# Kernel tuning notes

Hardware: AMD Instinct MI355X
Metric: run time of the kernel (lower is better)

## Reference

```python
import jax, jax.numpy as jnp
import numpy as np

HIDDEN = 896
NUM_Q_HEADS = 14
NUM_KV_HEADS = 2
HEAD_DIM = 64
ROPE_BASE = 10000.0
B, S = 4, 2048


def rotate_half(x):
    x1, x2 = jnp.split(x, 2, axis=-1)
    return jnp.concatenate((-x2, x1), axis=-1)


def rope_cos_sin(position_ids):
    # position_ids: [B, S] int -> cos/sin [B, 1, S, HEAD_DIM]
    inv_freq = 1.0 / (ROPE_BASE ** (jnp.arange(0, HEAD_DIM, 2, dtype=jnp.float32) / HEAD_DIM))
    freqs = position_ids.astype(jnp.float32)[..., None] * inv_freq  # [B,S,D/2]
    emb = jnp.concatenate((freqs, freqs), axis=-1)  # [B,S,D]
    return jnp.cos(emb)[:, None, :, :], jnp.sin(emb)[:, None, :, :]


def setup_inputs() -> dict:
    key = jax.random.key(0)
    k1, k2, k3, k4, k5 = jax.random.split(key, 5)
    s = 1.0 / np.sqrt(HIDDEN)
    return {
        "hidden_states": jax.random.normal(k1, (B, S, HIDDEN), dtype=jnp.float32),
        "position_ids": jnp.broadcast_to(jnp.arange(S, dtype=jnp.int64), (B, S)),
        "Wq": jax.random.normal(k2, (HIDDEN, NUM_Q_HEADS * HEAD_DIM), dtype=jnp.float32) * s,
        "Wk": jax.random.normal(k3, (HIDDEN, NUM_KV_HEADS * HEAD_DIM), dtype=jnp.float32) * s,
        "Wv": jax.random.normal(k4, (HIDDEN, NUM_KV_HEADS * HEAD_DIM), dtype=jnp.float32) * s,
        "Wo": jax.random.normal(k5, (NUM_Q_HEADS * HEAD_DIM, HIDDEN), dtype=jnp.float32) * s,
    }


def reference(hidden_states, position_ids, Wq, Wk, Wv, Wo):
    b, s, _ = hidden_states.shape
    n_rep = NUM_Q_HEADS // NUM_KV_HEADS

    q = (hidden_states @ Wq).reshape(b, s, NUM_Q_HEADS, HEAD_DIM).transpose(0, 2, 1, 3)   # [B,Hq,S,D]
    k = (hidden_states @ Wk).reshape(b, s, NUM_KV_HEADS, HEAD_DIM).transpose(0, 2, 1, 3)  # [B,Hkv,S,D]
    v = (hidden_states @ Wv).reshape(b, s, NUM_KV_HEADS, HEAD_DIM).transpose(0, 2, 1, 3)

    cos, sin = rope_cos_sin(position_ids)  # [B,1,S,D]
    q = q * cos + rotate_half(q) * sin
    k = k * cos + rotate_half(k) * sin

    # repeat_interleave KV heads to match query heads
    k = jnp.repeat(k, n_rep, axis=1)  # [B,Hq,S,D]
    v = jnp.repeat(v, n_rep, axis=1)

    scale = 1.0 / jnp.sqrt(jnp.float32(HEAD_DIM))
    attn = jnp.einsum('bhqd,bhkd->bhqk', q, k) * scale  # [B,Hq,S,S]
    attn = jax.nn.softmax(attn, axis=-1)
    out = jnp.einsum('bhqk,bhkd->bhqd', attn, v)  # [B,Hq,S,D]
    out = out.transpose(0, 2, 1, 3).reshape(b, s, NUM_Q_HEADS * HEAD_DIM)
    return out @ Wo
```

## Files before the change

### kernel.cpp

```cpp
#include <hip/hip_runtime.h>
#include <hip/hip_bf16.h>
#include <math.h>

typedef unsigned short ushort_t;
typedef __bf16 bf16x8 __attribute__((ext_vector_type(8)));
typedef float f32x4 __attribute__((ext_vector_type(4)));

#define HIDDEN 896
#define NQH 14
#define NKVH 2
#define HD 64
#define SEQ 2048
#define NBATCH 4

__device__ inline ushort_t f2bf(float x) {
  union { float f; unsigned u; } c; c.f = x;
  unsigned r = c.u + 0x7FFFu + ((c.u >> 16) & 1u);
  return (ushort_t)(r >> 16);
}

__device__ inline unsigned pack2bf(float a, float b) {
  union { float f; unsigned u; } ca, cb; ca.f = a; cb.f = b;
  unsigned ua = ca.u + 0x8000u, ub = cb.u + 0x8000u;
  return __builtin_amdgcn_perm(ub, ua, 0x07060302);
}

__device__ inline unsigned cvtpk(float a, float b) {
  unsigned r;
  asm("v_cvt_pk_bf16_f32 %0, %1, %2" : "=v"(r) : "v"(a), "v"(b));
  return r;
}

__device__ inline bf16x8 ldfrag(const ushort_t* p) {
  return *reinterpret_cast<const bf16x8*>(p);
}

__device__ inline void async16(const ushort_t* g, ushort_t* l) {
  __builtin_amdgcn_global_load_lds(
      (const __attribute__((address_space(1))) void*)g,
      (__attribute__((address_space(3))) void*)l, 16, 0, 0);
}


__device__ inline void transpose_sec(const float* __restrict__ in, ushort_t* __restrict__ out,
                                     int K, int N, int bx, int by) {
  __shared__ float tile[32][33];
  int k0 = by * 32, n0 = bx * 32;
  for (int r = threadIdx.y; r < 32; r += 8) {
    int k = k0 + r, n = n0 + threadIdx.x;
    tile[r][threadIdx.x] = (k < K && n < N) ? in[(size_t)k * N + n] : 0.f;
  }
  __syncthreads();
  for (int r = threadIdx.y; r < 32; r += 8) {
    int n = n0 + r, k = k0 + threadIdx.x;
    if (n < N && k < K) out[(size_t)n * K + k] = f2bf(tile[threadIdx.x][r]);
  }
}

__global__ void k_prep(const float* __restrict__ hidden, ushort_t* __restrict__ hb,
                       const float* __restrict__ Wq, const float* __restrict__ Wk,
                       const float* __restrict__ Wv, const float* __restrict__ Wo,
                       ushort_t* __restrict__ wT, ushort_t* __restrict__ woT,
                       float2* __restrict__ ctab) {
  const int blk = blockIdx.x;
  const int tid = threadIdx.y * 32 + threadIdx.x;
  if (blk < 7168) {
    int i = blk * 256 + tid;
    float4 v = reinterpret_cast<const float4*>(hidden)[i];
    ushort4 o;
    o.x = f2bf(v.x); o.y = f2bf(v.y); o.z = f2bf(v.z); o.w = f2bf(v.w);
    reinterpret_cast<ushort4*>(hb)[i] = o;
  } else if (blk < 7424) {
    int idx = (blk - 7168) * 256 + tid;
    int s = idx >> 5, dp = idx & 31;
    float inv = exp2f(-(float)dp * 0.41524101186092596f);
    float ang = (float)s * inv;
    float sn, cn;
    sincosf(ang, &sn, &cn);
    ctab[idx] = make_float2(cn, sn);
  } else if (blk < 8208) {
    int t = blk - 7424;
    transpose_sec(Wq, wT, 896, 896, t % 28, t / 28);
  } else if (blk < 8320) {
    int t = blk - 8208;
    transpose_sec(Wk, wT + (size_t)896 * 896, 896, 128, t % 4, t / 4);
  } else if (blk < 8432) {
    int t = blk - 8320;
    transpose_sec(Wv, wT + (size_t)1024 * 896, 896, 128, t % 4, t / 4);
  } else {
    int t = blk - 8432;
    transpose_sec(Wo, woT, 896, 896, t % 28, t / 28);
  }
}

__global__ __launch_bounds__(256) void k_qkv(
    const ushort_t* __restrict__ hb,
    const ushort_t* __restrict__ wT,
    const int* __restrict__ pos_ids,
    const float2* __restrict__ ctab,
    ushort_t* __restrict__ Qg,
    ushort_t* __restrict__ Kg,
    ushort_t* __restrict__ Vtg) {
  __shared__ ushort_t smem[12288];
  ushort_t* sa = smem;
  ushort_t* sbb = smem + 8192;

  const int f = blockIdx.x;
  const int x = f & 7, s8 = f >> 3;
  const int sect = s8 % 18;
  const int mt = (s8 / 18) * 8 + x;
  const int nt0 = sect * 64;
  const int m0 = mt * 128;
  const int tid = threadIdx.x;
  const int wave = tid >> 6, lane = tid & 63;
  const int l15 = lane & 15, quad = lane >> 4;
  const int sw = l15 & 7;

  f32x4 acc[2][4];
  const f32x4 z4 = {0.f, 0.f, 0.f, 0.f};
#pragma unroll
  for (int mm = 0; mm < 2; ++mm)
#pragma unroll
    for (int nb = 0; nb < 4; ++nb) acc[mm][nb] = z4;

  for (int kt = 0; kt < 14; ++kt) {
    const int k0 = kt * 64;
    __syncthreads();
#pragma unroll
    for (int i = 0; i < 4; ++i) {
      int id = i * 256 + tid;
      int row = id >> 3;
      int cs = (id & 7) ^ (row & 7);
      async16(hb + (size_t)(m0 + row) * HIDDEN + k0 + cs * 8, sa + (i * 256 + wave * 64) * 8);
    }
#pragma unroll
    for (int i = 0; i < 2; ++i) {
      int id = i * 256 + tid;
      int row = id >> 3;
      int cs = (id & 7) ^ (row & 7);
      async16(wT + (size_t)(nt0 + row) * HIDDEN + k0 + cs * 8, sbb + (i * 256 + wave * 64) * 8);
    }
    __syncthreads();
#pragma unroll
    for (int kc = 0; kc < 2; ++kc) {
      int c = kc * 4 + quad;
      bf16x8 af[2], bf[4];
#pragma unroll
      for (int mm = 0; mm < 2; ++mm)
        af[mm] = ldfrag(sa + ((wave * 32 + mm * 16 + l15) * 8 + (c ^ sw)) * 8);
#pragma unroll
      for (int nb = 0; nb < 4; ++nb)
        bf[nb] = ldfrag(sbb + ((nb * 16 + l15) * 8 + (c ^ sw)) * 8);
#pragma unroll
      for (int mm = 0; mm < 2; ++mm)
#pragma unroll
        for (int nb = 0; nb < 4; ++nb)
          acc[mm][nb] = __builtin_amdgcn_mfma_f32_16x16x32_bf16(af[mm], bf[nb], acc[mm][nb], 0, 0, 0);
    }
  }

  if (sect < 16) {
    const bool isQ = sect < 14;
    const float csc = isQ ? 0.125f * 1.4426950408889634f : 1.0f;
    ushort_t* dst = isQ ? Qg : Kg;
    const int nheads = isQ ? NQH : NKVH;
    const int hh = isQ ? sect : sect - 14;
#pragma unroll
    for (int mm = 0; mm < 2; ++mm) {
#pragma unroll
      for (int r = 0; r < 4; ++r) {
        int token = m0 + wave * 32 + mm * 16 + quad * 4 + r;
        int b = token >> 11, s = token & 2047;
        int pos = pos_ids[token];
        size_t base = ((size_t)(b * nheads + hh) * SEQ + s) * HD;
#pragma unroll
        for (int nb = 0; nb < 2; ++nb) {
          float2 cs = ctab[pos * 32 + nb * 16 + l15];
          float x0 = acc[mm][nb][r];
          float x1 = acc[mm][nb + 2][r];
          float y0 = (x0 * cs.x - x1 * cs.y) * csc;
          float y1 = (x1 * cs.x + x0 * cs.y) * csc;
          dst[base + nb * 16 + l15]      = f2bf(y0);
          dst[base + nb * 16 + l15 + 32] = f2bf(y1);
        }
      }
    }
  } else {
    const int kvh = sect - 16;
    __syncthreads();
    ushort_t* vt = smem;
#pragma unroll
    for (int mm = 0; mm < 2; ++mm) {
      int tl = wave * 32 + mm * 16 + quad * 4;
      int chunk = tl >> 3, ofs = tl & 7;
#pragma unroll
      for (int nb = 0; nb < 4; ++nb) {
        int row = nb * 16 + l15;
        int slot = chunk ^ (row & 7);
        ushort_t* p = vt + row * 128 + slot * 8 + ofs;
        *reinterpret_cast<unsigned*>(p)     = pack2bf(acc[mm][nb][0], acc[mm][nb][1]);
        *reinterpret_cast<unsigned*>(p + 2) = pack2bf(acc[mm][nb][2], acc[mm][nb][3]);
      }
    }
    __syncthreads();
    const int bb = m0 >> 11, s0 = m0 & 2047;
#pragma unroll
    for (int i = 0; i < 4; ++i) {
      int id = i * 256 + tid;
      int row = id >> 4, ch = id & 15;
      int slot = ch ^ (row & 7);
      uint4 v = *reinterpret_cast<const uint4*>(vt + row * 128 + slot * 8);
      *reinterpret_cast<uint4*>(Vtg + ((size_t)(bb * NKVH + kvh) * HD + row) * SEQ + s0 + ch * 8) = v;
    }
  }
}

__global__ __launch_bounds__(256) void k_attn(
    const ushort_t* __restrict__ Qg,
    const ushort_t* __restrict__ Kg,
    const ushort_t* __restrict__ Vtg,
    ushort_t* __restrict__ attn) {
  __shared__ ushort_t kbuf[2][32 * 64];
  __shared__ ushort_t vbuf[2][64 * 32];
  __shared__ ushort_t pbuf[4][32 * 40];

  const int f = blockIdx.x;
  const int x = f & 7, s8 = f >> 3;
  const int lh = s8 % 7;
  const int qt = s8 / 7;
  const int b = x >> 1, kvh = x & 1;
  const int h = kvh * 7 + lh;
  const int bh = b * NQH + h;
  const int tid = threadIdx.x;
  const int wave = tid >> 6, lane = tid & 63;
  const int l15 = lane & 15, quad = lane >> 4;
  const int q0 = qt * 128;

  bf16x8 qf[2][2];
#pragma unroll
  for (int qs = 0; qs < 2; ++qs) {
    const size_t qb = ((size_t)bh * SEQ + q0 + wave * 32 + qs * 16 + l15) * HD + quad * 8;
    qf[qs][0] = ldfrag(Qg + qb);
    qf[qs][1] = ldfrag(Qg + qb + 32);
  }

  const size_t kbase = (size_t)(b * NKVH + kvh) * SEQ * HD;
  const size_t vbase = (size_t)(b * NKVH + kvh) * HD * SEQ;

  const int krow = tid >> 3;
  const int kcs = (tid & 7) ^ (krow & 7);
  const int vrow = tid >> 2;
  const int vcs = (tid & 3) ^ ((vrow >> 1) & 3);
  const int sdst = wave * 512;

  const ushort_t* kg = Kg + kbase + (size_t)krow * HD + kcs * 8;
  const ushort_t* vg = Vtg + vbase + (size_t)vrow * SEQ + vcs * 8;

  float l_part[2] = {0.f, 0.f};
  f32x4 o[2][4];
  const f32x4 z4 = {0.f, 0.f, 0.f, 0.f};
#pragma unroll
  for (int qs = 0; qs < 2; ++qs)
#pragma unroll
    for (int nb = 0; nb < 4; ++nb) o[qs][nb] = z4;

  ushort_t* pw = pbuf[wave];

  auto stage = [&](ushort_t* kb, ushort_t* vb) {
    async16(kg, kb + sdst);
    async16(vg, vb + sdst);
    kg += 32 * HD;
    vg += 32;
  };

  auto compute = [&](const ushort_t* kb, const ushort_t* vb) {
#pragma unroll
    for (int nb = 0; nb < 2; ++nb) {
      int row = nb * 16 + l15;
      int swz = row & 7;
      bf16x8 kf0 = ldfrag(kb + (row * 8 + (quad ^ swz)) * 8);
      bf16x8 kf1 = ldfrag(kb + (row * 8 + ((4 + quad) ^ swz)) * 8);
#pragma unroll
      for (int qs = 0; qs < 2; ++qs) {
        f32x4 t = z4;
        t = __builtin_amdgcn_mfma_f32_16x16x32_bf16(kf0, qf[qs][0], t, 0, 0, 0);
        t = __builtin_amdgcn_mfma_f32_16x16x32_bf16(kf1, qf[qs][1], t, 0, 0, 0);
        float p0 = __builtin_amdgcn_exp2f(t[0]);
        float p1 = __builtin_amdgcn_exp2f(t[1]);
        float p2 = __builtin_amdgcn_exp2f(t[2]);
        float p3 = __builtin_amdgcn_exp2f(t[3]);
        l_part[qs] += (p0 + p1) + (p2 + p3);
        uint2 d;
        d.x = cvtpk(p0, p1);
        d.y = cvtpk(p2, p3);
        *reinterpret_cast<uint2*>(pw + (qs * 16 + l15) * 40 + nb * 16 + quad * 4) = d;
      }
    }

    bf16x8 pf[2];
#pragma unroll
    for (int qs = 0; qs < 2; ++qs)
      pf[qs] = ldfrag(pw + (qs * 16 + l15) * 40 + quad * 8);
#pragma unroll
    for (int nb = 0; nb < 4; ++nb) {
      int row = nb * 16 + l15;
      bf16x8 vf = ldfrag(vb + row * 32 + ((quad ^ ((row >> 1) & 3)) * 8));
#pragma unroll
      for (int qs = 0; qs < 2; ++qs)
        o[qs][nb] = __builtin_amdgcn_mfma_f32_16x16x32_bf16(pf[qs], vf, o[qs][nb], 0, 0, 0);
    }
  };

  stage(kbuf[0], vbuf[0]);
  asm volatile("s_waitcnt vmcnt(0)" ::: "memory");
  __builtin_amdgcn_s_barrier();
  __builtin_amdgcn_sched_barrier(0);

  for (int jt = 0; jt < 62; jt += 2) {
    stage(kbuf[1], vbuf[1]);
    compute(kbuf[0], vbuf[0]);
    __builtin_amdgcn_sched_barrier(0);
    asm volatile("s_waitcnt vmcnt(0)" ::: "memory");
    __builtin_amdgcn_s_barrier();
    __builtin_amdgcn_sched_barrier(0);

    stage(kbuf[0], vbuf[0]);
    compute(kbuf[1], vbuf[1]);
    __builtin_amdgcn_sched_barrier(0);
    asm volatile("s_waitcnt vmcnt(0)" ::: "memory");
    __builtin_amdgcn_s_barrier();
    __builtin_amdgcn_sched_barrier(0);
  }
  stage(kbuf[1], vbuf[1]);
  compute(kbuf[0], vbuf[0]);
  __builtin_amdgcn_sched_barrier(0);
  asm volatile("s_waitcnt vmcnt(0)" ::: "memory");
  __builtin_amdgcn_s_barrier();
  __builtin_amdgcn_sched_barrier(0);
  compute(kbuf[1], vbuf[1]);

#pragma unroll
  for (int qs = 0; qs < 2; ++qs) {
    float s = l_part[qs];
    s += __shfl_xor(s, 16);
    s += __shfl_xor(s, 32);
    l_part[qs] = s;
  }

#pragma unroll
  for (int qs = 0; qs < 2; ++qs) {
    float il = 1.0f / l_part[qs];
#pragma unroll
    for (int r = 0; r < 4; ++r) {
      float inv = __shfl(il, quad * 4 + r);
      int qg = q0 + wave * 32 + qs * 16 + quad * 4 + r;
#pragma unroll
      for (int nb = 0; nb < 4; ++nb) {
        float val = o[qs][nb][r] * inv;
        attn[(size_t)(b * SEQ + qg) * (NQH * HD) + h * HD + nb * 16 + l15] = f2bf(val);
      }
    }
  }
}

__global__ __launch_bounds__(256) void k_oproj(
    const ushort_t* __restrict__ attn,
    const ushort_t* __restrict__ woT,
    float* __restrict__ out) {
  __shared__ ushort_t smem[12288];
  ushort_t* sa = smem;
  ushort_t* sbb = smem + 8192;

  const int f = blockIdx.x;
  const int x = f & 7, s8 = f >> 3;
  const int n_sect = s8 % 14;
  const int mt = (s8 / 14) * 8 + x;
  const int n0 = n_sect * 64;
  const int m0 = mt * 128;
  const int tid = threadIdx.x;
  const int wave = tid >> 6, lane = tid & 63;
  const int l15 = lane & 15, quad = lane >> 4;
  const int sw = l15 & 7;

  f32x4 acc[2][4];
  const f32x4 z4 = {0.f, 0.f, 0.f, 0.f};
#pragma unroll
  for (int mm = 0; mm < 2; ++mm)
#pragma unroll
    for (int nb = 0; nb < 4; ++nb) acc[mm][nb] = z4;

  for (int kt = 0; kt < 14; ++kt) {
    const int k0 = kt * 64;
    __syncthreads();
#pragma unroll
    for (int i = 0; i < 4; ++i) {
      int id = i * 256 + tid;
      int row = id >> 3;
      int cs = (id & 7) ^ (row & 7);
      async16(attn + (size_t)(m0 + row) * HIDDEN + k0 + cs * 8, sa + (i * 256 + wave * 64) * 8);
    }
#pragma unroll
    for (int i = 0; i < 2; ++i) {
      int id = i * 256 + tid;
      int row = id >> 3;
      int cs = (id & 7) ^ (row & 7);
      async16(woT + (size_t)(n0 + row) * HIDDEN + k0 + cs * 8, sbb + (i * 256 + wave * 64) * 8);
    }
    __syncthreads();
#pragma unroll
    for (int kc = 0; kc < 2; ++kc) {
      int c = kc * 4 + quad;
      bf16x8 af[2], bf[4];
#pragma unroll
      for (int mm = 0; mm < 2; ++mm)
        af[mm] = ldfrag(sa + ((wave * 32 + mm * 16 + l15) * 8 + (c ^ sw)) * 8);
#pragma unroll
      for (int nb = 0; nb < 4; ++nb)
        bf[nb] = ldfrag(sbb + ((nb * 16 + l15) * 8 + (c ^ sw)) * 8);
#pragma unroll
      for (int mm = 0; mm < 2; ++mm)
#pragma unroll
        for (int nb = 0; nb < 4; ++nb)
          acc[mm][nb] = __builtin_amdgcn_mfma_f32_16x16x32_bf16(af[mm], bf[nb], acc[mm][nb], 0, 0, 0);
    }
  }

#pragma unroll
  for (int mm = 0; mm < 2; ++mm)
#pragma unroll
    for (int nb = 0; nb < 4; ++nb)
#pragma unroll
      for (int r = 0; r < 4; ++r)
        out[(size_t)(m0 + wave * 32 + mm * 16 + quad * 4 + r) * HIDDEN +
            n0 + nb * 16 + l15] = acc[mm][nb][r];
}


extern "C" void kernel_launch(void* const* d_in, const int* in_sizes, int n_in,
                              void* d_out, int out_size, void* d_ws, size_t ws_size,
                              hipStream_t stream) {
  (void)in_sizes; (void)n_in; (void)out_size; (void)ws_size;
  const float* hidden = (const float*)d_in[0];
  const int* pos      = (const int*)d_in[1];
  const float* Wq     = (const float*)d_in[2];
  const float* Wk     = (const float*)d_in[3];
  const float* Wv     = (const float*)d_in[4];
  const float* Wo     = (const float*)d_in[5];
  float* out = (float*)d_out;

  char* ws = (char*)d_ws;
  ushort_t* hb   = (ushort_t*)(ws);
  ushort_t* wT   = (ushort_t*)(ws + 14680064);
  float2*   ctab = (float2*)  (ws + 16744448);
  ushort_t* Qg   = (ushort_t*)(ws + 17268736);
  ushort_t* Kg   = (ushort_t*)(ws + 31948800);
  ushort_t* Vtg  = (ushort_t*)(ws + 34045952);
  ushort_t* attn = (ushort_t*)(ws + 36143104);
  ushort_t* woT  = (ushort_t*)(ws + 50823168);

  k_prep<<<9216, dim3(32, 8), 0, stream>>>(hidden, hb, Wq, Wk, Wv, Wo, wT, woT, ctab);
  k_qkv<<<1152, 256, 0, stream>>>(hb, wT, pos, ctab, Qg, Kg, Vtg);
  k_attn<<<896, 256, 0, stream>>>(Qg, Kg, Vtg, attn);
  k_oproj<<<896, 256, 0, stream>>>(attn, woT, out);
}
```

Baseline: 223.5 us.

## Triple-buffer async K-loop in QKV and output projection GEMMs

Both projection GEMMs now use a K-tile of 32 with three shared-memory buffers. Global-to-LDS async copies for the next tiles are issued before computing the current one, and each step waits with a partial vmcnt count and a single barrier, replacing the old load-all-then-compute loop with two barriers per tile. The LDS swizzle is adapted to the narrower 32-wide rows. The last stage re-issues a duplicate load so the vmcnt counting stays uniform. This costs more LDS per block and relies on hand-placed waitcnt and sched barriers for correctness.

Result: slower. 229.7 us (+2.8%).

```diff
diff --git a/kernel.cpp b/kernel.cpp
--- a/kernel.cpp
+++ b/kernel.cpp
@@ -101,9 +101,7 @@
     ushort_t* __restrict__ Qg,
     ushort_t* __restrict__ Kg,
     ushort_t* __restrict__ Vtg) {
-  __shared__ ushort_t smem[12288];
-  ushort_t* sa = smem;
-  ushort_t* sbb = smem + 8192;
+  __shared__ ushort_t smem[18432];
 
   const int f = blockIdx.x;
   const int x = f & 7, s8 = f >> 3;
@@ -114,7 +112,7 @@
   const int tid = threadIdx.x;
   const int wave = tid >> 6, lane = tid & 63;
   const int l15 = lane & 15, quad = lane >> 4;
-  const int sw = l15 & 7;
+  const int c4 = quad ^ ((l15 >> 1) & 3);
 
   f32x4 acc[2][4];
   const f32x4 z4 = {0.f, 0.f, 0.f, 0.f};
@@ -123,41 +121,64 @@
 #pragma unroll
     for (int nb = 0; nb < 4; ++nb) acc[mm][nb] = z4;
 
-  for (int kt = 0; kt < 14; ++kt) {
-    const int k0 = kt * 64;
-    __syncthreads();
-#pragma unroll
-    for (int i = 0; i < 4; ++i) {
-      int id = i * 256 + tid;
-      int row = id >> 3;
-      int cs = (id & 7) ^ (row & 7);
-      async16(hb + (size_t)(m0 + row) * HIDDEN + k0 + cs * 8, sa + (i * 256 + wave * 64) * 8);
-    }
-#pragma unroll
-    for (int i = 0; i < 2; ++i) {
-      int id = i * 256 + tid;
-      int row = id >> 3;
-      int cs = (id & 7) ^ (row & 7);
-      async16(wT + (size_t)(nt0 + row) * HIDDEN + k0 + cs * 8, sbb + (i * 256 + wave * 64) * 8);
-    }
-    __syncthreads();
-#pragma unroll
-    for (int kc = 0; kc < 2; ++kc) {
-      int c = kc * 4 + quad;
-      bf16x8 af[2], bf[4];
-#pragma unroll
-      for (int mm = 0; mm < 2; ++mm)
-        af[mm] = ldfrag(sa + ((wave * 32 + mm * 16 + l15) * 8 + (c ^ sw)) * 8);
+  const int cA1 = 256 + tid;
+  const int rA0 = tid >> 2,  sA0 = (tid & 3) ^ ((rA0 >> 1) & 3);
+  const int rA1 = cA1 >> 2,  sA1 = (cA1 & 3) ^ ((rA1 >> 1) & 3);
+  const int rB  = tid >> 2,  sB  = (tid & 3) ^ ((rB >> 1) & 3);
+  const ushort_t* pA0 = hb + (size_t)(m0 + rA0) * HIDDEN + sA0 * 8;
+  const ushort_t* pA1 = hb + (size_t)(m0 + rA1) * HIDDEN + sA1 * 8;
+  const ushort_t* pB  = wT + (size_t)(nt0 + rB) * HIDDEN + sB * 8;
+  const int dA0 = (wave * 64) * 8;
+  const int dA1 = 2048 + (wave * 64) * 8;
+  const int dB  = 4096 + (wave * 64) * 8;
+
+  ushort_t* const b0 = smem;
+  ushort_t* const b1 = smem + 6144;
+  ushort_t* const b2 = smem + 12288;
+
+  auto stage = [&](int off, ushort_t* buf) {
+    async16(pA0 + off, buf + dA0);
+    async16(pA1 + off, buf + dA1);
+    async16(pB + off, buf + dB);
+  };
+
+  auto compute = [&](const ushort_t* buf) {
+    bf16x8 af[2], bf[4];
+#pragma unroll
+    for (int mm = 0; mm < 2; ++mm)
+      af[mm] = ldfrag(buf + (wave * 32 + mm * 16 + l15) * 32 + c4 * 8);
+#pragma unroll
+    for (int nb = 0; nb < 4; ++nb)
+      bf[nb] = ldfrag(buf + 4096 + (nb * 16 + l15) * 32 + c4 * 8);
+#pragma unroll
+    for (int mm = 0; mm < 2; ++mm)
 #pragma unroll
       for (int nb = 0; nb < 4; ++nb)
-        bf[nb] = ldfrag(sbb + ((nb * 16 + l15) * 8 + (c ^ sw)) * 8);
-#pragma unroll
-      for (int mm = 0; mm < 2; ++mm)
-#pragma unroll
-        for (int nb = 0; nb < 4; ++nb)
-          acc[mm][nb] = __builtin_amdgcn_mfma_f32_16x16x32_bf16(af[mm], bf[nb], acc[mm][nb], 0, 0, 0);
-    }
-  }
+        acc[mm][nb] = __builtin_amdgcn_mfma_f32_16x16x32_bf16(af[mm], bf[nb], acc[mm][nb], 0, 0, 0);
+  };
+
+#define QKV_SYNC() \
+  __builtin_amdgcn_sched_barrier(0); \
+  asm volatile("s_waitcnt vmcnt(3)" ::: "memory"); \
+  __builtin_amdgcn_s_barrier(); \
+  __builtin_amdgcn_sched_barrier(0);
+
+  stage(0, b0);
+  stage(32, b1);
+  QKV_SYNC();
+  pA0 += 64; pA1 += 64; pB += 64;
+
+  for (int i = 0; i < 8; ++i) {
+    stage(0, b2);  compute(b0);  QKV_SYNC();
+    stage(32, b0); compute(b1);  QKV_SYNC();
+    stage(64, b1); compute(b2);  QKV_SYNC();
+    pA0 += 96; pA1 += 96; pB += 96;
+  }
+  stage(0, b2);  compute(b0);  QKV_SYNC();
+  stage(32, b0); compute(b1);  QKV_SYNC();
+  stage(32, b1); compute(b2);  QKV_SYNC();
+  compute(b0);
+#undef QKV_SYNC
 
   if (sect < 16) {
     const bool isQ = sect < 14;
@@ -187,6 +208,7 @@
     }
   } else {
     const int kvh = sect - 16;
+    asm volatile("s_waitcnt vmcnt(0)" ::: "memory");
     __syncthreads();
     ushort_t* vt = smem;
 #pragma unroll
@@ -367,9 +389,7 @@
     const ushort_t* __restrict__ attn,
     const ushort_t* __restrict__ woT,
     float* __restrict__ out) {
-  __shared__ ushort_t smem[12288];
-  ushort_t* sa = smem;
-  ushort_t* sbb = smem + 8192;
+  __shared__ ushort_t smem[18432];
 
   const int f = blockIdx.x;
   const int x = f & 7, s8 = f >> 3;
@@ -380,7 +400,7 @@
   const int tid = threadIdx.x;
   const int wave = tid >> 6, lane = tid & 63;
   const int l15 = lane & 15, quad = lane >> 4;
-  const int sw = l15 & 7;
+  const int c4 = quad ^ ((l15 >> 1) & 3);
 
   f32x4 acc[2][4];
   const f32x4 z4 = {0.f, 0.f, 0.f, 0.f};
@@ -389,41 +409,64 @@
 #pragma unroll
     for (int nb = 0; nb < 4; ++nb) acc[mm][nb] = z4;
 
-  for (int kt = 0; kt < 14; ++kt) {
-    const int k0 = kt * 64;
-    __syncthreads();
-#pragma unroll
-    for (int i = 0; i < 4; ++i) {
-      int id = i * 256 + tid;
-      int row = id >> 3;
-      int cs = (id & 7) ^ (row & 7);
-      async16(attn + (size_t)(m0 + row) * HIDDEN + k0 + cs * 8, sa + (i * 256 + wave * 64) * 8);
-    }
-#pragma unroll
-    for (int i = 0; i < 2; ++i) {
-      int id = i * 256 + tid;
-      int row = id >> 3;
-      int cs = (id & 7) ^ (row & 7);
-      async16(woT + (size_t)(n0 + row) * HIDDEN + k0 + cs * 8, sbb + (i * 256 + wave * 64) * 8);
-    }
-    __syncthreads();
-#pragma unroll
-    for (int kc = 0; kc < 2; ++kc) {
-      int c = kc * 4 + quad;
-      bf16x8 af[2], bf[4];
-#pragma unroll
-      for (int mm = 0; mm < 2; ++mm)
-        af[mm] = ldfrag(sa + ((wave * 32 + mm * 16 + l15) * 8 + (c ^ sw)) * 8);
+  const int cA1 = 256 + tid;
+  const int rA0 = tid >> 2,  sA0 = (tid & 3) ^ ((rA0 >> 1) & 3);
+  const int rA1 = cA1 >> 2,  sA1 = (cA1 & 3) ^ ((rA1 >> 1) & 3);
+  const int rB  = tid >> 2,  sB  = (tid & 3) ^ ((rB >> 1) & 3);
+  const ushort_t* pA0 = attn + (size_t)(m0 + rA0) * HIDDEN + sA0 * 8;
+  const ushort_t* pA1 = attn + (size_t)(m0 + rA1) * HIDDEN + sA1 * 8;
+  const ushort_t* pB  = woT + (size_t)(n0 + rB) * HIDDEN + sB * 8;
+  const int dA0 = (wave * 64) * 8;
+  const int dA1 = 2048 + (wave * 64) * 8;
+  const int dB  = 4096 + (wave * 64) * 8;
+
+  ushort_t* const b0 = smem;
+  ushort_t* const b1 = smem + 6144;
+  ushort_t* const b2 = smem + 12288;
+
+  auto stage = [&](int off, ushort_t* buf) {
+    async16(pA0 + off, buf + dA0);
+    async16(pA1 + off, buf + dA1);
+    async16(pB + off, buf + dB);
+  };
+
+  auto compute = [&](const ushort_t* buf) {
+    bf16x8 af[2], bf[4];
+#pragma unroll
+    for (int mm = 0; mm < 2; ++mm)
+      af[mm] = ldfrag(buf + (wave * 32 + mm * 16 + l15) * 32 + c4 * 8);
+#pragma unroll
+    for (int nb = 0; nb < 4; ++nb)
+      bf[nb] = ldfrag(buf + 4096 + (nb * 16 + l15) * 32 + c4 * 8);
+#pragma unroll
+    for (int mm = 0; mm < 2; ++mm)
 #pragma unroll
       for (int nb = 0; nb < 4; ++nb)
-        bf[nb] = ldfrag(sbb + ((nb * 16 + l15) * 8 + (c ^ sw)) * 8);
-#pragma unroll
-      for (int mm = 0; mm < 2; ++mm)
-#pragma unroll
-        for (int nb = 0; nb < 4; ++nb)
-          acc[mm][nb] = __builtin_amdgcn_mfma_f32_16x16x32_bf16(af[mm], bf[nb], acc[mm][nb], 0, 0, 0);
-    }
-  }
+        acc[mm][nb] = __builtin_amdgcn_mfma_f32_16x16x32_bf16(af[mm], bf[nb], acc[mm][nb], 0, 0, 0);
+  };
+
+#define OPJ_SYNC() \
+  __builtin_amdgcn_sched_barrier(0); \
+  asm volatile("s_waitcnt vmcnt(3)" ::: "memory"); \
+  __builtin_amdgcn_s_barrier(); \
+  __builtin_amdgcn_sched_barrier(0);
+
+  stage(0, b0);
+  stage(32, b1);
+  OPJ_SYNC();
+  pA0 += 64; pA1 += 64; pB += 64;
+
+  for (int i = 0; i < 8; ++i) {
+    stage(0, b2);  compute(b0);  OPJ_SYNC();
+    stage(32, b0); compute(b1);  OPJ_SYNC();
+    stage(64, b1); compute(b2);  OPJ_SYNC();
+    pA0 += 96; pA1 += 96; pB += 96;
+  }
+  stage(0, b2);  compute(b0);  OPJ_SYNC();
+  stage(32, b0); compute(b1);  OPJ_SYNC();
+  stage(32, b1); compute(b2);  OPJ_SYNC();
+  compute(b0);
+#undef OPJ_SYNC
 
 #pragma unroll
   for (int mm = 0; mm < 2; ++mm)
```
